# Kernel optimization log

Measured on AMD Instinct MI355X. Metric: run time of the kernel, lower is better.

Reference implementation:

```python
import jax, jax.numpy as jnp
import numpy as np

D_MODEL = 1024
NUM_HEADS = 16
D_K = D_MODEL // NUM_HEADS
B, S = 4, 2048


def setup_inputs() -> dict:
    key = jax.random.key(0)
    ks = jax.random.split(key, 7)
    scale = 1.0 / np.sqrt(D_MODEL)
    return {
        "q": jax.random.normal(ks[0], (B, S, D_MODEL), jnp.float32),
        "k": jax.random.normal(ks[1], (B, S, D_MODEL), jnp.float32),
        "v": jax.random.normal(ks[2], (B, S, D_MODEL), jnp.float32),
        "w_q": jax.random.normal(ks[3], (D_MODEL, D_MODEL), jnp.float32) * scale,
        "w_k": jax.random.normal(ks[4], (D_MODEL, D_MODEL), jnp.float32) * scale,
        "w_v": jax.random.normal(ks[5], (D_MODEL, D_MODEL), jnp.float32) * scale,
        "w_o": jax.random.normal(ks[6], (D_MODEL, D_MODEL), jnp.float32) * scale,
    }


def reference(q, k, v, w_q, w_k, w_v, w_o):
    # projections: [B,S,D] @ [D,D]
    qh = (q @ w_q).reshape(B, -1, NUM_HEADS, D_K).transpose(0, 2, 1, 3)  # [B,H,S,dk]
    kh = (k @ w_k).reshape(B, -1, NUM_HEADS, D_K).transpose(0, 2, 1, 3)
    vh = (v @ w_v).reshape(B, -1, NUM_HEADS, D_K).transpose(0, 2, 1, 3)
    scores = jnp.einsum("bhqd,bhkd->bhqk", qh, kh) / jnp.sqrt(jnp.float32(D_K))
    attn = jax.nn.softmax(scores, axis=-1)  # dropout is identity in eval mode
    out = jnp.einsum("bhqk,bhkd->bhqd", attn, vh)  # [B,H,S,dk]
    out = out.transpose(0, 2, 1, 3).reshape(B, -1, D_MODEL)
    return out @ w_o, attn
```

## Files before the change

### kernel.cpp

```cpp
#include <hip/hip_runtime.h>


typedef __attribute__((ext_vector_type(8))) short bf16x8;
typedef __attribute__((ext_vector_type(4))) float f32x4;
typedef __attribute__((ext_vector_type(8))) unsigned short u16x8;
typedef __attribute__((ext_vector_type(4))) unsigned int u32x4;

#define L2E 1.4426950408889634f

__device__ __forceinline__ unsigned short f2bf(float x) {
    unsigned u = __float_as_uint(x);
    u += 0x7FFFu + ((u >> 16) & 1u);
    return (unsigned short)(u >> 16);
}

__device__ __forceinline__ uint2 pk4(f32x4 v) {
    unsigned r0, r1;
    asm("v_cvt_pk_bf16_f32 %0, %1, %2" : "=v"(r0) : "v"(v[0]), "v"(v[1]));
    asm("v_cvt_pk_bf16_f32 %0, %1, %2" : "=v"(r1) : "v"(v[2]), "v"(v[3]));
    return make_uint2(r0, r1);
}

__device__ __forceinline__ void gll16(const void* g, void* l) {
    __builtin_amdgcn_global_load_lds(
        (const __attribute__((address_space(1))) void*)g,
        (__attribute__((address_space(3))) void*)l, 16, 0, 0);
}

__global__ __launch_bounds__(256) void cvt3(
    const float* __restrict__ q, const float* __restrict__ k, const float* __restrict__ v,
    unsigned short* __restrict__ qb, unsigned short* __restrict__ kb, unsigned short* __restrict__ vb)
{
    int b = blockIdx.x;
    int which = b >> 12;
    const float* src = which == 0 ? q : (which == 1 ? k : v);
    unsigned short* dst = which == 0 ? qb : (which == 1 ? kb : vb);
    size_t off = ((size_t)(b & 4095) * 256 + threadIdx.x) * 8;
    float4 x0 = *(const float4*)(src + off);
    float4 x1 = *(const float4*)(src + off + 4);
    u16x8 o;
    o[0] = f2bf(x0.x); o[1] = f2bf(x0.y); o[2] = f2bf(x0.z); o[3] = f2bf(x0.w);
    o[4] = f2bf(x1.x); o[5] = f2bf(x1.y); o[6] = f2bf(x1.z); o[7] = f2bf(x1.w);
    *(u16x8*)(dst + off) = o;
}

__global__ __launch_bounds__(256) void wtrans(
    const float* __restrict__ w0, const float* __restrict__ w1,
    const float* __restrict__ w2, const float* __restrict__ w3,
    unsigned short* __restrict__ o0, unsigned short* __restrict__ o1,
    unsigned short* __restrict__ o2, unsigned short* __restrict__ o3)
{
    __shared__ float T[64 * 68];
    int b = blockIdx.x;
    int wi = b >> 8, tile = b & 255;
    int k0 = (tile >> 4) * 64, n0 = (tile & 15) * 64;
    const float* W = wi == 0 ? w0 : (wi == 1 ? w1 : (wi == 2 ? w2 : w3));
    unsigned short* O = wi == 0 ? o0 : (wi == 1 ? o1 : (wi == 2 ? o2 : o3));
    float scale = (wi == 0) ? 0.125f : 1.0f;
    int t = threadIdx.x;
#pragma unroll
    for (int i = 0; i < 4; i++) {
        int idx = i * 256 + t;
        int r = idx >> 4, ch = idx & 15;
        float4 vv = *(const float4*)(W + (size_t)(k0 + r) * 1024 + n0 + ch * 4);
        *(float4*)(&T[r * 68 + ch * 4]) = vv;
    }
    __syncthreads();
#pragma unroll
    for (int i = 0; i < 2; i++) {
        int idx = i * 256 + t;
        int n = idx >> 3, ch = idx & 7;
        u16x8 o;
#pragma unroll
        for (int jj = 0; jj < 8; jj++) o[jj] = f2bf(T[(ch * 8 + jj) * 68 + n] * scale);
        *(u16x8*)(O + (size_t)(n0 + n) * 1024 + k0 + ch * 8) = o;
    }
}

template<int MODE>
__global__ __launch_bounds__(256) void gemm128(
    const unsigned short* __restrict__ A0, const unsigned short* __restrict__ A1, const unsigned short* __restrict__ A2,
    const unsigned short* __restrict__ B0, const unsigned short* __restrict__ B1, const unsigned short* __restrict__ B2,
    void* O0, void* O1, void* O2)
{
    constexpr int K = 1024, NK = 32;
    __shared__ unsigned short As[2][128 * 32];
    __shared__ unsigned short Bs[2][128 * 32];
    const int t = threadIdx.x, lane = t & 63, w = t >> 6;
    const int z = blockIdx.z;
    const unsigned short* A  = z == 0 ? A0 : (z == 1 ? A1 : A2);
    const unsigned short* Bt = z == 0 ? B0 : (z == 1 ? B1 : B2);
    void* O = z == 0 ? O0 : (z == 1 ? O1 : O2);
    const bool vt = (MODE == 0) && (z == 2);
    int bid = blockIdx.x;
    int xcd = bid & 7, seq = bid >> 3;
    int npan = seq >> 3, mpan = ((seq & 7) << 3) + xcd;
    int m0 = mpan * 128, n0 = npan * 128;
    int wr = w >> 1, wc = w & 1;
    int qhi = lane >> 4, rr = lane & 15;

    auto stage = [&](int buf, int kt) {
#pragma unroll
        for (int i = 0; i < 2; i++) {
            int o = ((w * 2 + i) << 10) + (lane << 4);
            int r = o >> 6, c = o & 63;
            int sc = c ^ (((r >> 1) & 3) << 4);
            gll16((const char*)A + ((size_t)(m0 + r) * K + kt * 32) * 2 + sc,
                  (char*)&As[buf][0] + ((w * 2 + i) << 10));
        }
#pragma unroll
        for (int i = 0; i < 2; i++) {
            int o = ((w * 2 + i) << 10) + (lane << 4);
            int r = o >> 6, c = o & 63;
            int sc = c ^ (((r >> 1) & 3) << 4);
            gll16((const char*)Bt + ((size_t)(n0 + r) * K + kt * 32) * 2 + sc,
                  (char*)&Bs[buf][0] + ((w * 2 + i) << 10));
        }
    };

    f32x4 acc[4][4] = {};
    stage(0, 0);
    __syncthreads();
    int buf = 0;
    for (int kt = 0; kt < NK; kt++) {
        if (kt + 1 < NK) stage(buf ^ 1, kt + 1);
        const char* as = (const char*)&As[buf][0];
        const char* bs = (const char*)&Bs[buf][0];
        bf16x8 a[4], b[4];
#pragma unroll
        for (int mi = 0; mi < 4; mi++) {
            int r = wr * 64 + mi * 16 + rr;
            a[mi] = *(const bf16x8*)(as + r * 64 + ((qhi << 4) ^ (((r >> 1) & 3) << 4)));
        }
#pragma unroll
        for (int ni = 0; ni < 4; ni++) {
            int r = wc * 64 + ni * 16 + rr;
            b[ni] = *(const bf16x8*)(bs + r * 64 + ((qhi << 4) ^ (((r >> 1) & 3) << 4)));
        }
        if (vt) {
#pragma unroll
            for (int mi = 0; mi < 4; mi++)
#pragma unroll
                for (int ni = 0; ni < 4; ni++)
                    acc[mi][ni] = __builtin_amdgcn_mfma_f32_16x16x32_bf16(a[mi], b[ni], acc[mi][ni], 0, 0, 0);
        } else {
#pragma unroll
            for (int mi = 0; mi < 4; mi++)
#pragma unroll
                for (int ni = 0; ni < 4; ni++)
                    acc[mi][ni] = __builtin_amdgcn_mfma_f32_16x16x32_bf16(b[ni], a[mi], acc[mi][ni], 0, 0, 0);
        }
        __syncthreads();
        buf ^= 1;
    }

    if (MODE == 1) {
#pragma unroll
        for (int mi = 0; mi < 4; mi++) {
            int m = m0 + wr * 64 + mi * 16 + rr;
#pragma unroll
            for (int ni = 0; ni < 4; ni++) {
                int n = n0 + wc * 64 + ni * 16 + qhi * 4;
                f32x4 o = acc[mi][ni];
                __builtin_nontemporal_store(o, (f32x4*)((float*)O + (size_t)m * 1024 + n));
            }
        }
    } else if (vt) {
        unsigned short* Vt = (unsigned short*)O;
#pragma unroll
        for (int mi = 0; mi < 4; mi++) {
            int m = m0 + wr * 64 + mi * 16 + qhi * 4;
#pragma unroll
            for (int ni = 0; ni < 4; ni++) {
                int n = n0 + wc * 64 + ni * 16 + rr;
                int bh = (m >> 11) * 16 + (n >> 6);
                *(uint2*)(Vt + ((size_t)bh * 64 + (n & 63)) * 2048 + (m & 2047)) = pk4(acc[mi][ni]);
            }
        }
    } else {
        unsigned short* Oh = (unsigned short*)O;
#pragma unroll
        for (int mi = 0; mi < 4; mi++) {
            int m = m0 + wr * 64 + mi * 16 + rr;
#pragma unroll
            for (int ni = 0; ni < 4; ni++) {
                int n = n0 + wc * 64 + ni * 16 + qhi * 4;
                size_t idx = (((size_t)((m >> 11) * 16 + (n >> 6))) * 2048 + (m & 2047)) * 64 + (n & 63);
                *(uint2*)(Oh + idx) = pk4(acc[mi][ni]);
            }
        }
    }
}

__global__ __launch_bounds__(256) void attn64(
    const unsigned short* __restrict__ Qh, const unsigned short* __restrict__ Kh,
    const unsigned short* __restrict__ Vt, float* __restrict__ attn,
    unsigned short* __restrict__ ctx)
{
    __shared__ unsigned short Ks[2][64 * 64];
    __shared__ unsigned short Vs[2][64 * 64];
    __shared__ float St[4][1024];
    const int t = threadIdx.x, lane = t & 63, w = t >> 6;
    int bid = blockIdx.x;
    int rm = (bid & 7) * 256 + (bid >> 3);
    int bh = rm >> 5, rb = rm & 31;
    int qhi = lane >> 4, rr = lane & 15;
    int q0 = rb * 64 + w * 16;

    const unsigned short* qb = Qh + ((size_t)bh * 2048 + q0 + rr) * 64;
    bf16x8 aq0 = *(const bf16x8*)(qb + qhi * 8);
    bf16x8 aq1 = *(const bf16x8*)(qb + 32 + qhi * 8);

    auto stageK = [&](int buf, int ct) {
#pragma unroll
        for (int i = 0; i < 2; i++) {
            int o = ((w * 2 + i) << 10) + (lane << 4);
            int r = o >> 7, c = o & 127;
            int sc = c ^ ((r & 7) << 4);
            gll16((const char*)Kh + (size_t)(bh * 2048 + ct * 64 + r) * 128 + sc,
                  (char*)&Ks[buf][0] + ((w * 2 + i) << 10));
        }
    };
    auto stageV = [&](int buf, int ct) {
#pragma unroll
        for (int i = 0; i < 2; i++) {
            int o = ((w * 2 + i) << 10) + (lane << 4);
            int r = o >> 7, c = o & 127;
            int sc = c ^ ((r & 7) << 4);
            gll16((const char*)Vt + (size_t)(bh * 64 + r) * 4096 + ct * 128 + sc,
                  (char*)&Vs[buf][0] + ((w * 2 + i) << 10));
        }
    };

    f32x4 sv = {0.f, 0.f, 0.f, 0.f};
    stageK(0, 0);
    __syncthreads();
    int buf = 0;
    for (int ct = 0; ct < 32; ct++) {
        if (ct < 31) stageK(buf ^ 1, ct + 1);
        const char* ks = (const char*)&Ks[buf][0];
#pragma unroll
        for (int n = 0; n < 4; n++) {
            int r = n * 16 + rr;
            int sw = (r & 7) << 4;
            bf16x8 b0 = *(const bf16x8*)(ks + r * 128 + ((qhi << 4) ^ sw));
            bf16x8 b1 = *(const bf16x8*)(ks + r * 128 + ((64 | (qhi << 4)) ^ sw));
            f32x4 z4 = {0.f, 0.f, 0.f, 0.f};
            f32x4 s = __builtin_amdgcn_mfma_f32_16x16x32_bf16(b0, aq0, z4, 0, 0, 0);
            s = __builtin_amdgcn_mfma_f32_16x16x32_bf16(b1, aq1, s, 0, 0, 0);
#pragma unroll
            for (int j = 0; j < 4; j++) sv[j] += exp2f(s[j] * L2E);
        }
        __syncthreads();
        buf ^= 1;
    }
    float lsum = sv[0] + sv[1] + sv[2] + sv[3];
    lsum += __shfl_xor(lsum, 16);
    lsum += __shfl_xor(lsum, 32);
    float lr2 = -__log2f(lsum);

    stageK(0, 0); stageV(0, 0);
    __syncthreads();
    buf = 0;
    float* ab = attn + (size_t)bh * 2048 * 2048;
    float* stw = &St[w][0];
    f32x4 acco[4] = {};
    for (int ct = 0; ct < 32; ct++) {
        if (ct < 31) { stageK(buf ^ 1, ct + 1); stageV(buf ^ 1, ct + 1); }
        const char* ks = (const char*)&Ks[buf][0];
        f32x4 s[4];
#pragma unroll
        for (int n = 0; n < 4; n++) {
            int r = n * 16 + rr;
            int sw = (r & 7) << 4;
            bf16x8 b0 = *(const bf16x8*)(ks + r * 128 + ((qhi << 4) ^ sw));
            bf16x8 b1 = *(const bf16x8*)(ks + r * 128 + ((64 | (qhi << 4)) ^ sw));
            f32x4 z4 = {0.f, 0.f, 0.f, 0.f};
            s[n] = __builtin_amdgcn_mfma_f32_16x16x32_bf16(b0, aq0, z4, 0, 0, 0);
            s[n] = __builtin_amdgcn_mfma_f32_16x16x32_bf16(b1, aq1, s[n], 0, 0, 0);
        }
        unsigned wA[4], wB[4];
#pragma unroll
        for (int n = 0; n < 4; n++) {
            f32x4 pv;
#pragma unroll
            for (int j = 0; j < 4; j++) pv[j] = exp2f(s[n][j] * L2E + lr2);
            *(f32x4*)(stw + rr * 64 + (((n * 4 + qhi) ^ rr) << 2)) = pv;
            asm("v_cvt_pk_bf16_f32 %0, %1, %2" : "=v"(wA[n]) : "v"(pv[0]), "v"(pv[1]));
            asm("v_cvt_pk_bf16_f32 %0, %1, %2" : "=v"(wB[n]) : "v"(pv[2]), "v"(pv[3]));
        }
        const char* vs = (const char*)&Vs[buf][0];
#pragma unroll
        for (int kb = 0; kb < 2; kb++) {
            u32x4 fw = {wA[2 * kb], wB[2 * kb], wA[2 * kb + 1], wB[2 * kb + 1]};
            bf16x8 pf = *(bf16x8*)&fw;
#pragma unroll
            for (int db = 0; db < 4; db++) {
                int r = db * 16 + rr;
                int sw = (r & 7) << 4;
                uint2 lo8 = *(const uint2*)(vs + r * 128 + ((kb * 64 + qhi * 8) ^ sw));
                uint2 hi8 = *(const uint2*)(vs + r * 128 + ((kb * 64 + 32 + qhi * 8) ^ sw));
                u32x4 vw = {lo8.x, lo8.y, hi8.x, hi8.y};
                bf16x8 vf = *(bf16x8*)&vw;
                acco[db] = __builtin_amdgcn_mfma_f32_16x16x32_bf16(vf, pf, acco[db], 0, 0, 0);
            }
        }
#pragma unroll
        for (int i = 0; i < 4; i++) {
            int r = 4 * i + qhi;
            f32x4 vvv = *(const f32x4*)(stw + r * 64 + ((rr ^ r) << 2));
            __builtin_nontemporal_store(vvv,
                (f32x4*)(ab + (size_t)(q0 + r) * 2048 + ct * 64 + rr * 4));
        }
        asm volatile("s_waitcnt vmcnt(4)" ::: "memory");
        __builtin_amdgcn_s_barrier();
        buf ^= 1;
    }
    int b_ = bh >> 4, h_ = bh & 15;
    unsigned short* cw = ctx + ((size_t)b_ * 2048 + q0 + rr) * 1024 + h_ * 64;
#pragma unroll
    for (int db = 0; db < 4; db++)
        *(uint2*)(cw + db * 16 + qhi * 4) = pk4(acco[db]);
}

extern "C" void kernel_launch(void* const* d_in, const int* in_sizes, int n_in,
                              void* d_out, int out_size, void* d_ws, size_t ws_size,
                              hipStream_t stream)
{
    (void)in_sizes; (void)n_in; (void)out_size; (void)ws_size;
    const float* q  = (const float*)d_in[0];
    const float* k  = (const float*)d_in[1];
    const float* v  = (const float*)d_in[2];
    const float* wq = (const float*)d_in[3];
    const float* wk = (const float*)d_in[4];
    const float* wv = (const float*)d_in[5];
    const float* wo = (const float*)d_in[6];
    char* ws = (char*)d_ws;
    const size_t M1 = 1ull << 20;
    unsigned short* qbf = (unsigned short*)(ws);
    unsigned short* kbf = (unsigned short*)(ws + 16 * M1);
    unsigned short* vbf = (unsigned short*)(ws + 32 * M1);
    unsigned short* wqt = (unsigned short*)(ws + 48 * M1);
    unsigned short* wkt = (unsigned short*)(ws + 50 * M1);
    unsigned short* wvt = (unsigned short*)(ws + 52 * M1);
    unsigned short* wot = (unsigned short*)(ws + 54 * M1);
    unsigned short* Qh  = (unsigned short*)(ws + 56 * M1);
    unsigned short* Kh  = (unsigned short*)(ws + 72 * M1);
    unsigned short* Vt  = (unsigned short*)(ws + 88 * M1);
    unsigned short* ctx = kbf;
    float* out0 = (float*)d_out;
    float* attn = out0 + (size_t)8192 * 1024;

    cvt3<<<12288, 256, 0, stream>>>(q, k, v, qbf, kbf, vbf);
    wtrans<<<1024, 256, 0, stream>>>(wq, wk, wv, wo, wqt, wkt, wvt, wot);
    gemm128<0><<<dim3(512, 1, 3), 256, 0, stream>>>(qbf, kbf, vbf, wqt, wkt, wvt,
                                                    (void*)Qh, (void*)Kh, (void*)Vt);
    attn64<<<2048, 256, 0, stream>>>(Qh, Kh, Vt, attn, ctx);
    gemm128<1><<<dim3(512, 1, 1), 256, 0, stream>>>(ctx, ctx, ctx, wot, wot, wot,
                                                    (void*)out0, (void*)out0, (void*)out0);
}
```

Baseline: 414.3 us.

## Process two query tiles per attention block, fusing second tile's row-sum into first pass

The attention kernel now handles 128 query rows per block in two 64-row halves. The row-sum (softmax denominator) pass for the second half is folded into the output pass of the first half, so three sweeps over K replace four. The log2(e) factor is also folded into the Q weight scale, which removes a multiply per exponential. Register pressure rises from holding two sets of Q fragments, and the grid is halved to 1024 blocks with a 3-block occupancy hint.

```diff
diff --git a/kernel.cpp b/kernel.cpp
--- a/kernel.cpp
+++ b/kernel.cpp
@@ -5,8 +5,6 @@
 typedef __attribute__((ext_vector_type(4))) float f32x4;
 typedef __attribute__((ext_vector_type(8))) unsigned short u16x8;
 typedef __attribute__((ext_vector_type(4))) unsigned int u32x4;
-
-#define L2E 1.4426950408889634f
 
 __device__ __forceinline__ unsigned short f2bf(float x) {
     unsigned u = __float_as_uint(x);
@@ -56,7 +54,7 @@
     int k0 = (tile >> 4) * 64, n0 = (tile & 15) * 64;
     const float* W = wi == 0 ? w0 : (wi == 1 ? w1 : (wi == 2 ? w2 : w3));
     unsigned short* O = wi == 0 ? o0 : (wi == 1 ? o1 : (wi == 2 ? o2 : o3));
-    float scale = (wi == 0) ? 0.125f : 1.0f;
+    float scale = (wi == 0) ? 0.18033688011112042f : 1.0f;
     int t = threadIdx.x;
 #pragma unroll
     for (int i = 0; i < 4; i++) {
@@ -192,7 +190,7 @@
     }
 }
 
-__global__ __launch_bounds__(256) void attn64(
+__global__ __launch_bounds__(256, 3) void attn2(
     const unsigned short* __restrict__ Qh, const unsigned short* __restrict__ Kh,
     const unsigned short* __restrict__ Vt, float* __restrict__ attn,
     unsigned short* __restrict__ ctx)
@@ -202,14 +200,18 @@
     __shared__ float St[4][1024];
     const int t = threadIdx.x, lane = t & 63, w = t >> 6;
     int bid = blockIdx.x;
-    int rm = (bid & 7) * 256 + (bid >> 3);
-    int bh = rm >> 5, rb = rm & 31;
+    int rm = (bid & 7) * 128 + (bid >> 3);
+    int bh = rm >> 4, rb = rm & 15;
     int qhi = lane >> 4, rr = lane & 15;
-    int q0 = rb * 64 + w * 16;
-
-    const unsigned short* qb = Qh + ((size_t)bh * 2048 + q0 + rr) * 64;
-    bf16x8 aq0 = *(const bf16x8*)(qb + qhi * 8);
-    bf16x8 aq1 = *(const bf16x8*)(qb + 32 + qhi * 8);
+    int q00 = rb * 128 + w * 16;
+    int q01 = q00 + 64;
+
+    const unsigned short* qb0 = Qh + ((size_t)bh * 2048 + q00 + rr) * 64;
+    const unsigned short* qb1 = Qh + ((size_t)bh * 2048 + q01 + rr) * 64;
+    bf16x8 aqA0 = *(const bf16x8*)(qb0 + qhi * 8);
+    bf16x8 aqA1 = *(const bf16x8*)(qb0 + 32 + qhi * 8);
+    bf16x8 aqB0 = *(const bf16x8*)(qb1 + qhi * 8);
+    bf16x8 aqB1 = *(const bf16x8*)(qb1 + 32 + qhi * 8);
 
     auto stageK = [&](int buf, int ct) {
 #pragma unroll
@@ -231,6 +233,9 @@
                   (char*)&Vs[buf][0] + ((w * 2 + i) << 10));
         }
     };
+
+    float* ab = attn + (size_t)bh * 2048 * 2048;
+    float* stw = &St[w][0];
 
     f32x4 sv = {0.f, 0.f, 0.f, 0.f};
     stageK(0, 0);
@@ -246,10 +251,10 @@
             bf16x8 b0 = *(const bf16x8*)(ks + r * 128 + ((qhi << 4) ^ sw));
             bf16x8 b1 = *(const bf16x8*)(ks + r * 128 + ((64 | (qhi << 4)) ^ sw));
             f32x4 z4 = {0.f, 0.f, 0.f, 0.f};
-            f32x4 s = __builtin_amdgcn_mfma_f32_16x16x32_bf16(b0, aq0, z4, 0, 0, 0);
-            s = __builtin_amdgcn_mfma_f32_16x16x32_bf16(b1, aq1, s, 0, 0, 0);
-#pragma unroll
-            for (int j = 0; j < 4; j++) sv[j] += exp2f(s[j] * L2E);
+            f32x4 s = __builtin_amdgcn_mfma_f32_16x16x32_bf16(b0, aqA0, z4, 0, 0, 0);
+            s = __builtin_amdgcn_mfma_f32_16x16x32_bf16(b1, aqA1, s, 0, 0, 0);
+#pragma unroll
+            for (int j = 0; j < 4; j++) sv[j] += exp2f(s[j]);
         }
         __syncthreads();
         buf ^= 1;
@@ -257,18 +262,17 @@
     float lsum = sv[0] + sv[1] + sv[2] + sv[3];
     lsum += __shfl_xor(lsum, 16);
     lsum += __shfl_xor(lsum, 32);
-    float lr2 = -__log2f(lsum);
-
+    float lr2a = -__log2f(lsum);
+
+    f32x4 sv1 = {0.f, 0.f, 0.f, 0.f};
+    f32x4 acco[4] = {};
     stageK(0, 0); stageV(0, 0);
     __syncthreads();
     buf = 0;
-    float* ab = attn + (size_t)bh * 2048 * 2048;
-    float* stw = &St[w][0];
-    f32x4 acco[4] = {};
     for (int ct = 0; ct < 32; ct++) {
         if (ct < 31) { stageK(buf ^ 1, ct + 1); stageV(buf ^ 1, ct + 1); }
         const char* ks = (const char*)&Ks[buf][0];
-        f32x4 s[4];
+        f32x4 s0[4];
 #pragma unroll
         for (int n = 0; n < 4; n++) {
             int r = n * 16 + rr;
@@ -276,15 +280,19 @@
             bf16x8 b0 = *(const bf16x8*)(ks + r * 128 + ((qhi << 4) ^ sw));
             bf16x8 b1 = *(const bf16x8*)(ks + r * 128 + ((64 | (qhi << 4)) ^ sw));
             f32x4 z4 = {0.f, 0.f, 0.f, 0.f};
-            s[n] = __builtin_amdgcn_mfma_f32_16x16x32_bf16(b0, aq0, z4, 0, 0, 0);
-            s[n] = __builtin_amdgcn_mfma_f32_16x16x32_bf16(b1, aq1, s[n], 0, 0, 0);
+            s0[n] = __builtin_amdgcn_mfma_f32_16x16x32_bf16(b0, aqA0, z4, 0, 0, 0);
+            s0[n] = __builtin_amdgcn_mfma_f32_16x16x32_bf16(b1, aqA1, s0[n], 0, 0, 0);
+            f32x4 s1 = __builtin_amdgcn_mfma_f32_16x16x32_bf16(b0, aqB0, z4, 0, 0, 0);
+            s1 = __builtin_amdgcn_mfma_f32_16x16x32_bf16(b1, aqB1, s1, 0, 0, 0);
+#pragma unroll
+            for (int j = 0; j < 4; j++) sv1[j] += exp2f(s1[j]);
         }
         unsigned wA[4], wB[4];
 #pragma unroll
         for (int n = 0; n < 4; n++) {
             f32x4 pv;
 #pragma unroll
-            for (int j = 0; j < 4; j++) pv[j] = exp2f(s[n][j] * L2E + lr2);
+            for (int j = 0; j < 4; j++) pv[j] = exp2f(s0[n][j] + lr2a);
             *(f32x4*)(stw + rr * 64 + (((n * 4 + qhi) ^ rr) << 2)) = pv;
             asm("v_cvt_pk_bf16_f32 %0, %1, %2" : "=v"(wA[n]) : "v"(pv[0]), "v"(pv[1]));
             asm("v_cvt_pk_bf16_f32 %0, %1, %2" : "=v"(wB[n]) : "v"(pv[2]), "v"(pv[3]));
@@ -310,17 +318,86 @@
             int r = 4 * i + qhi;
             f32x4 vvv = *(const f32x4*)(stw + r * 64 + ((rr ^ r) << 2));
             __builtin_nontemporal_store(vvv,
-                (f32x4*)(ab + (size_t)(q0 + r) * 2048 + ct * 64 + rr * 4));
+                (f32x4*)(ab + (size_t)(q00 + r) * 2048 + ct * 64 + rr * 4));
         }
         asm volatile("s_waitcnt vmcnt(4)" ::: "memory");
         __builtin_amdgcn_s_barrier();
         buf ^= 1;
     }
     int b_ = bh >> 4, h_ = bh & 15;
-    unsigned short* cw = ctx + ((size_t)b_ * 2048 + q0 + rr) * 1024 + h_ * 64;
-#pragma unroll
-    for (int db = 0; db < 4; db++)
-        *(uint2*)(cw + db * 16 + qhi * 4) = pk4(acco[db]);
+    {
+        unsigned short* cw = ctx + ((size_t)b_ * 2048 + q00 + rr) * 1024 + h_ * 64;
+#pragma unroll
+        for (int db = 0; db < 4; db++)
+            *(uint2*)(cw + db * 16 + qhi * 4) = pk4(acco[db]);
+    }
+    float lsum1 = sv1[0] + sv1[1] + sv1[2] + sv1[3];
+    lsum1 += __shfl_xor(lsum1, 16);
+    lsum1 += __shfl_xor(lsum1, 32);
+    float lr2b = -__log2f(lsum1);
+
+#pragma unroll
+    for (int db = 0; db < 4; db++) acco[db] = (f32x4){0.f, 0.f, 0.f, 0.f};
+    stageK(0, 0); stageV(0, 0);
+    __syncthreads();
+    buf = 0;
+    for (int ct = 0; ct < 32; ct++) {
+        if (ct < 31) { stageK(buf ^ 1, ct + 1); stageV(buf ^ 1, ct + 1); }
+        const char* ks = (const char*)&Ks[buf][0];
+        f32x4 s[4];
+#pragma unroll
+        for (int n = 0; n < 4; n++) {
+            int r = n * 16 + rr;
+            int sw = (r & 7) << 4;
+            bf16x8 b0 = *(const bf16x8*)(ks + r * 128 + ((qhi << 4) ^ sw));
+            bf16x8 b1 = *(const bf16x8*)(ks + r * 128 + ((64 | (qhi << 4)) ^ sw));
+            f32x4 z4 = {0.f, 0.f, 0.f, 0.f};
+            s[n] = __builtin_amdgcn_mfma_f32_16x16x32_bf16(b0, aqB0, z4, 0, 0, 0);
+            s[n] = __builtin_amdgcn_mfma_f32_16x16x32_bf16(b1, aqB1, s[n], 0, 0, 0);
+        }
+        unsigned wA[4], wB[4];
+#pragma unroll
+        for (int n = 0; n < 4; n++) {
+            f32x4 pv;
+#pragma unroll
+            for (int j = 0; j < 4; j++) pv[j] = exp2f(s[n][j] + lr2b);
+            *(f32x4*)(stw + rr * 64 + (((n * 4 + qhi) ^ rr) << 2)) = pv;
+            asm("v_cvt_pk_bf16_f32 %0, %1, %2" : "=v"(wA[n]) : "v"(pv[0]), "v"(pv[1]));
+            asm("v_cvt_pk_bf16_f32 %0, %1, %2" : "=v"(wB[n]) : "v"(pv[2]), "v"(pv[3]));
+        }
+        const char* vs = (const char*)&Vs[buf][0];
+#pragma unroll
+        for (int kb = 0; kb < 2; kb++) {
+            u32x4 fw = {wA[2 * kb], wB[2 * kb], wA[2 * kb + 1], wB[2 * kb + 1]};
+            bf16x8 pf = *(bf16x8*)&fw;
+#pragma unroll
+            for (int db = 0; db < 4; db++) {
+                int r = db * 16 + rr;
+                int sw = (r & 7) << 4;
+                uint2 lo8 = *(const uint2*)(vs + r * 128 + ((kb * 64 + qhi * 8) ^ sw));
+                uint2 hi8 = *(const uint2*)(vs + r * 128 + ((kb * 64 + 32 + qhi * 8) ^ sw));
+                u32x4 vw = {lo8.x, lo8.y, hi8.x, hi8.y};
+                bf16x8 vf = *(bf16x8*)&vw;
+                acco[db] = __builtin_amdgcn_mfma_f32_16x16x32_bf16(vf, pf, acco[db], 0, 0, 0);
+            }
+        }
+#pragma unroll
+        for (int i = 0; i < 4; i++) {
+            int r = 4 * i + qhi;
+            f32x4 vvv = *(const f32x4*)(stw + r * 64 + ((rr ^ r) << 2));
+            __builtin_nontemporal_store(vvv,
+                (f32x4*)(ab + (size_t)(q01 + r) * 2048 + ct * 64 + rr * 4));
+        }
+        asm volatile("s_waitcnt vmcnt(4)" ::: "memory");
+        __builtin_amdgcn_s_barrier();
+        buf ^= 1;
+    }
+    {
+        unsigned short* cw = ctx + ((size_t)b_ * 2048 + q01 + rr) * 1024 + h_ * 64;
+#pragma unroll
+        for (int db = 0; db < 4; db++)
+            *(uint2*)(cw + db * 16 + qhi * 4) = pk4(acco[db]);
+    }
 }
 
 extern "C" void kernel_launch(void* const* d_in, const int* in_sizes, int n_in,
@@ -355,7 +432,7 @@
     wtrans<<<1024, 256, 0, stream>>>(wq, wk, wv, wo, wqt, wkt, wvt, wot);
     gemm128<0><<<dim3(512, 1, 3), 256, 0, stream>>>(qbf, kbf, vbf, wqt, wkt, wvt,
                                                     (void*)Qh, (void*)Kh, (void*)Vt);
-    attn64<<<2048, 256, 0, stream>>>(Qh, Kh, Vt, attn, ctx);
+    attn2<<<1024, 256, 0, stream>>>(Qh, Kh, Vt, attn, ctx);
     gemm128<1><<<dim3(512, 1, 1), 256, 0, stream>>>(ctx, ctx, ctx, wot, wot, wot,
                                                     (void*)out0, (void*)out0, (void*)out0);
 }
```

Measured after the change: 405.2 us (median of 3 runs). -2.2%, faster.
